# Performance work log

Hardware: AMD Instinct MI355X
Metric: run time of the kernel (lower is better)

Reference implementation:

```python
import jax, jax.numpy as jnp
import numpy as np

D_MODEL = 1024
N_HEADS = 16
D_K = D_MODEL // N_HEADS
THETA = 10000.0
NEG_INF = -1e30


def _rope_tables(token_positions, d_k, theta=THETA):
    # freqs[t, i] = t / theta**(2i/d_k), i in [0, d_k/2)
    exponent = jnp.arange(0, d_k, 2, dtype=jnp.float32)  # [d_k/2]
    inv_freq = 1.0 / theta ** (exponent / d_k)
    freqs = token_positions.astype(jnp.float32)[:, None] * inv_freq[None, :]  # [s, d_k/2]
    return jnp.cos(freqs), jnp.sin(freqs)


def _apply_rope(x, cos, sin):
    # x: [..., s, d_k]; interleaved pair rotation (pairs are (x[2i], x[2i+1]))
    x1 = x[..., 0::2]
    x2 = x[..., 1::2]
    r1 = x1 * cos - x2 * sin
    r2 = x1 * sin + x2 * cos
    return jnp.stack([r1, r2], axis=-1).reshape(x.shape)


def setup_inputs() -> dict:
    key = jax.random.key(0)
    ks = jax.random.split(key, 5)
    b, s = 2, 2048
    scale = np.sqrt(2.0 / (D_MODEL + D_MODEL))
    return {
        "x": jax.random.normal(ks[0], (b, s, D_MODEL), dtype=jnp.float32),
        "Wq": jax.random.normal(ks[1], (D_MODEL, D_MODEL), dtype=jnp.float32) * scale,
        "Wk": jax.random.normal(ks[2], (D_MODEL, D_MODEL), dtype=jnp.float32) * scale,
        "Wv": jax.random.normal(ks[3], (D_MODEL, D_MODEL), dtype=jnp.float32) * scale,
        "Wo": jax.random.normal(ks[4], (D_MODEL, D_MODEL), dtype=jnp.float32) * scale,
        "token_positions": jnp.arange(s, dtype=jnp.int64 if jax.config.jax_enable_x64 else jnp.int32),
    }


def reference(x, Wq, Wk, Wv, Wo, token_positions):
    b, s, _ = x.shape
    # QKV projections: weight stored [in, out]
    q = jnp.einsum('bsi,io->bso', x, Wq)
    k = jnp.einsum('bsi,io->bso', x, Wk)
    v = jnp.einsum('bsi,io->bso', x, Wv)
    # split heads: [b, h, s, d_k]
    q = q.reshape(b, s, N_HEADS, D_K).transpose(0, 2, 1, 3)
    k = k.reshape(b, s, N_HEADS, D_K).transpose(0, 2, 1, 3)
    v = v.reshape(b, s, N_HEADS, D_K).transpose(0, 2, 1, 3)
    # RoPE
    cos, sin = _rope_tables(token_positions, D_K)
    q = _apply_rope(q, cos, sin)
    k = _apply_rope(k, cos, sin)
    # causal attention with full materialized scores (faithful to source)
    scores = jnp.einsum('bhid,bhjd->bhij', q, k) / jnp.sqrt(jnp.float32(D_K))
    mask = jnp.tril(jnp.ones((s, s), dtype=bool))
    scores = jnp.where(mask, scores, NEG_INF)
    probs = jax.nn.softmax(scores, axis=-1)
    out = jnp.einsum('bhij,bhjd->bhid', probs, v)
    out = out.transpose(0, 2, 1, 3).reshape(b, s, D_MODEL)
    return jnp.einsum('bsi,io->bso', out, Wo)
```

## Files before the change

### kernel.cpp

```cpp
#include <hip/hip_runtime.h>
#include <hip/hip_bf16.h>
#include <cmath>

#define S_LEN 2048
#define DMODEL 1024
#define NHEADS 16
#define DK 64
#define BATCH 2
#define MTOT (BATCH * S_LEN)

using short8 = __attribute__((ext_vector_type(8))) short;
using floatx4 = __attribute__((ext_vector_type(4))) float;

__device__ __forceinline__ unsigned short f2b(float f) {
    union { float f; unsigned u; } v; v.f = f;
    unsigned r = v.u + 0x7fff + ((v.u >> 16) & 1);
    return (unsigned short)(r >> 16);
}

__device__ __forceinline__ unsigned pack2(float a, float b) {
    float2 t; t.x = a; t.y = b;
    __hip_bfloat162 h = __float22bfloat162_rn(t);
    union { __hip_bfloat162 h; unsigned u; } v; v.h = h;
    return v.u;
}

__device__ __forceinline__ void gload16(const void* g, void* l) {
    __builtin_amdgcn_global_load_lds(
        (const __attribute__((address_space(1))) unsigned int*)g,
        (__attribute__((address_space(3))) unsigned int*)l, 16, 0, 0);
}

__global__ __launch_bounds__(256) void prep_k(
    const float* __restrict__ x, unsigned short* __restrict__ xb,
    const int* __restrict__ tokpos, float* __restrict__ ct, float* __restrict__ st,
    const float* W0, const float* W1, const float* W2, const float* W3,
    unsigned short* T0, unsigned short* T1, unsigned short* T2, unsigned short* T3) {
    __shared__ float t[64][65];
    const int b = blockIdx.x;
    if (b < 2048) {
        int i = (b * 256 + threadIdx.x) * 8;
        float4 a = *(const float4*)(x + i);
        float4 bb = *(const float4*)(x + i + 4);
        short8 o;
        o[0] = f2b(a.x); o[1] = f2b(a.y); o[2] = f2b(a.z); o[3] = f2b(a.w);
        o[4] = f2b(bb.x); o[5] = f2b(bb.y); o[6] = f2b(bb.z); o[7] = f2b(bb.w);
        *(short8*)(xb + i) = o;
    } else if (b < 2304) {
        int idx = (b - 2048) * 256 + threadIdx.x;
        int si = idx >> 5;
        int ip = idx & 31;
        float pos = (float)tokpos[si];
        float inv_freq = powf(10000.0f, -(float)(2 * ip) / 64.0f);
        float ang = pos * inv_freq;
        ct[idx] = cosf(ang);
        st[idx] = sinf(ang);
    } else {
        int id = b - 2304;
        int z = id >> 8;
        int bx = id & 15, by = (id >> 4) & 15;
        const float* W = z == 0 ? W0 : z == 1 ? W1 : z == 2 ? W2 : W3;
        unsigned short* T = z == 0 ? T0 : z == 1 ? T1 : z == 2 ? T2 : T3;
        const bool perm = (z < 2);
        int n0 = bx * 64, k0 = by * 64;
        int rr = threadIdx.x >> 6, cc = threadIdx.x & 63;
#pragma unroll
        for (int r = 0; r < 16; r++) {
            int row = r * 4 + rr;
            t[row][cc] = W[(size_t)(k0 + row) * DMODEL + n0 + cc];
        }
        __syncthreads();
#pragma unroll
        for (int r = 0; r < 16; r++) {
            int row = r * 4 + rr;
            int drow = perm ? (((row & 1) ? 32 : 0) + (row >> 1)) : row;
            T[(size_t)(n0 + drow) * DMODEL + k0 + cc] = f2b(t[cc][row]);
        }
    }
}

__global__ __launch_bounds__(256) void vtrans_k(const unsigned short* __restrict__ V,
                                                unsigned short* __restrict__ Vt) {
    __shared__ unsigned short t[64][72];
    const int tid = threadIdx.x;
    const int s0 = blockIdx.x * 64, d0 = blockIdx.y * 64;
    const int bb = s0 >> 11;
#pragma unroll
    for (int it = 0; it < 4; it++) {
        int e = (it * 256 + tid) * 4;
        int r = e >> 6, c = e & 63;
        *(ushort4*)&t[r][c] = *(const ushort4*)(V + (size_t)(s0 + r) * DMODEL + d0 + c);
    }
    __syncthreads();
#pragma unroll
    for (int it = 0; it < 4; it++) {
        int e = (it * 256 + tid) * 4;
        int r = e >> 6, c = e & 63;
        ushort4 v;
        v.x = t[c + 0][r]; v.y = t[c + 1][r];
        v.z = t[c + 2][r]; v.w = t[c + 3][r];
        *(ushort4*)(Vt + (size_t)(bb * 1024 + d0 + r) * S_LEN + (s0 & (S_LEN - 1)) + c) = v;
    }
}

__global__ __launch_bounds__(256) void mm_k(
    const unsigned short* __restrict__ A,
    const unsigned short* __restrict__ Bt0, const unsigned short* __restrict__ Bt1,
    const unsigned short* __restrict__ Bt2,
    void* C0, void* C1, void* C2,
    const float* __restrict__ ct, const float* __restrict__ st, int kind) {
    __shared__ __align__(16) unsigned short blob[2][8192];

    const int z = blockIdx.z;
    const unsigned short* Bt = z == 0 ? Bt0 : z == 1 ? Bt1 : Bt2;
    void* C = z == 0 ? C0 : z == 1 ? C1 : C2;
    const int mode = (kind == 1) ? 0 : (z == 2 ? 3 : 1);
    const float qscale = (z == 0 && kind == 0) ? 0.18033688011112042f : 1.0f;

    const int tid = threadIdx.x;
    const int w = tid >> 6, lane = tid & 63;
    const int l15 = lane & 15, quad = lane >> 4;
    const int wr = w >> 1, wc = w & 1;
    const int m0 = blockIdx.x * 128, n0 = blockIdx.y * 128;

    floatx4 acc[4][4];
#pragma unroll
    for (int i = 0; i < 4; i++)
#pragma unroll
        for (int j = 0; j < 4; j++) acc[i][j] = (floatx4){0.f, 0.f, 0.f, 0.f};

    auto stage = [&](int buf, int k0) {
#pragma unroll
        for (int it = 0; it < 4; it++) {
            int g = it * 4 + w;
            const unsigned short* gp;
            if (g < 8)
                gp = A + (size_t)(m0 + g * 16 + l15) * DMODEL + k0 + quad * 8;
            else
                gp = Bt + (size_t)(n0 + (g - 8) * 16 + l15) * DMODEL + k0 + quad * 8;
            gload16(gp, (char*)&blob[buf][0] + g * 1024);
        }
    };

    stage(0, 0);
    for (int kt = 0; kt < DMODEL / 32; kt++) {
        const int b = kt & 1;
        __syncthreads();
        if (kt + 1 < DMODEL / 32) stage(b ^ 1, (kt + 1) * 32);

        const char* base = (const char*)&blob[b][0];
        short8 af[4], bfr[4];
#pragma unroll
        for (int i = 0; i < 4; i++)
            af[i] = *(const short8*)(base + ((wr * 4 + i) * 64 + lane) * 16);
#pragma unroll
        for (int j = 0; j < 4; j++)
            bfr[j] = *(const short8*)(base + 8192 + ((wc * 4 + j) * 64 + lane) * 16);
#pragma unroll
        for (int i = 0; i < 4; i++)
#pragma unroll
            for (int j = 0; j < 4; j++)
                acc[i][j] = __builtin_amdgcn_mfma_f32_16x16x32_bf16(af[i], bfr[j], acc[i][j], 0, 0, 0);
    }

#pragma unroll
    for (int i = 0; i < 4; i++) {
        const int rowb = m0 + wr * 64 + i * 16 + quad * 4;
        if (mode == 0) {
            float* Cf = (float*)C;
#pragma unroll
            for (int j = 0; j < 4; j++) {
                int colb = n0 + wc * 64 + j * 16 + l15;
#pragma unroll
                for (int r = 0; r < 4; r++)
                    Cf[(size_t)(rowb + r) * DMODEL + colb] = acc[i][j][r];
            }
        } else if (mode == 1) {
            unsigned short* Cb = (unsigned short*)C;
#pragma unroll
            for (int jh = 0; jh < 2; jh++) {
                int ip = jh * 16 + l15;
                int cole = n0 + wc * 64 + jh * 16 + l15;
#pragma unroll
                for (int r = 0; r < 4; r++) {
                    int row = rowb + r;
                    int si = row & (S_LEN - 1);
                    float c = ct[si * 32 + ip] * qscale;
                    float s = st[si * 32 + ip] * qscale;
                    float e = acc[i][jh][r];
                    float od = acc[i][jh + 2][r];
                    Cb[(size_t)row * DMODEL + cole] = f2b(e * c - od * s);
                    Cb[(size_t)row * DMODEL + cole + 32] = f2b(e * s + od * c);
                }
            }
        } else {
            unsigned short* Cb = (unsigned short*)C;
#pragma unroll
            for (int j = 0; j < 4; j++) {
                int colb = n0 + wc * 64 + j * 16 + l15;
#pragma unroll
                for (int r = 0; r < 4; r++)
                    Cb[(size_t)(rowb + r) * DMODEL + colb] = f2b(acc[i][j][r]);
            }
        }
    }
}

__global__ __launch_bounds__(512) void attn_k(const unsigned short* __restrict__ Q,
                                              const unsigned short* __restrict__ K,
                                              const unsigned short* __restrict__ Vt,
                                              unsigned short* __restrict__ O) {
    __shared__ __align__(16) unsigned short Kblob[2][4096];
    __shared__ __align__(16) unsigned short Vblob[2][4096];
    __shared__ __align__(16) unsigned short Ps[8][16 * 72];

    const int tid = threadIdx.x;
    const int w = tid >> 6, lane = tid & 63;
    const int l15 = lane & 15, quad = lane >> 4;
    const int idx = blockIdx.x;
    const int qt = 15 - (idx >> 5);
    const int bh = idx & 31;
    const int bb = bh >> 4, h = bh & 15;
    const int qbase = qt * 128 + w * 16;
    const int qrow = qbase + l15;

    const size_t qoff = (size_t)(bb * S_LEN + qbase + l15) * DMODEL + h * DK;
    short8 aq0 = *(const short8*)(Q + qoff + quad * 8);
    short8 aq1 = *(const short8*)(Q + qoff + 32 + quad * 8);

    floatx4 o[4];
#pragma unroll
    for (int f = 0; f < 4; f++) o[f] = (floatx4){0.f, 0.f, 0.f, 0.f};
    float mv = -1e30f, lv = 0.f;

    const unsigned short* Kb = K + (size_t)(bb * S_LEN) * DMODEL + h * DK;
    const unsigned short* Vb = Vt + (size_t)(bb * 1024 + h * DK) * S_LEN;
    unsigned short* ps = &Ps[w][0];

    auto stage = [&](int b, int kb) {
#pragma unroll
        for (int it = 0; it < 2; it++) {
            int g = it * 8 + w;
            if (g < 8) {
                const unsigned short* gp =
                    Kb + (size_t)(kb + (g >> 1) * 16 + l15) * DMODEL + (g & 1) * 32 + quad * 8;
                gload16(gp, (char*)&Kblob[b][0] + g * 1024);
            } else {
                int gv = g - 8;
                const unsigned short* gp =
                    Vb + (size_t)((gv >> 1) * 16 + l15) * S_LEN + kb + (gv & 1) * 32 + quad * 8;
                gload16(gp, (char*)&Vblob[b][0] + gv * 1024);
            }
        }
    };

    const int nkt = 2 * qt + 2;
    stage(0, 0);
    for (int kt = 0; kt < nkt; kt++) {
        const int b = kt & 1;
        const int kb = kt * 64;
        __syncthreads();
        if (kt + 1 < nkt) stage(b ^ 1, (kt + 1) * 64);

        const unsigned short* kbb = &Kblob[b][0];
        floatx4 c[4];
#pragma unroll
        for (int g = 0; g < 4; g++) {
            short8 kf0 = *(const short8*)(kbb + (g * 2 + 0) * 512 + lane * 8);
            short8 kf1 = *(const short8*)(kbb + (g * 2 + 1) * 512 + lane * 8);
            floatx4 t = {0.f, 0.f, 0.f, 0.f};
            t = __builtin_amdgcn_mfma_f32_16x16x32_bf16(kf0, aq0, t, 0, 0, 0);
            c[g] = __builtin_amdgcn_mfma_f32_16x16x32_bf16(kf1, aq1, t, 0, 0, 0);
        }

        float sv[16];
        if (kb + 63 <= qbase) {
#pragma unroll
            for (int g = 0; g < 4; g++)
#pragma unroll
                for (int r = 0; r < 4; r++) sv[g * 4 + r] = c[g][r];
        } else {
#pragma unroll
            for (int g = 0; g < 4; g++)
#pragma unroll
                for (int r = 0; r < 4; r++) {
                    int key = kb + g * 16 + quad * 4 + r;
                    sv[g * 4 + r] = (key <= qrow) ? c[g][r] : -1e30f;
                }
        }
        float mx = sv[0];
#pragma unroll
        for (int i = 1; i < 16; i++) mx = fmaxf(mx, sv[i]);
        mx = fmaxf(mx, __shfl_xor(mx, 16));
        mx = fmaxf(mx, __shfl_xor(mx, 32));
        float mnew = fmaxf(mv, mx);
        float alpha = exp2f(mv - mnew);
        mv = mnew;
        float p[16], psum = 0.f;
#pragma unroll
        for (int i = 0; i < 16; i++) {
            p[i] = exp2f(sv[i] - mnew);
            psum += p[i];
        }
        lv = lv * alpha + psum;

#pragma unroll
        for (int g = 0; g < 4; g++) {
            uint2 pk;
            pk.x = pack2(p[g * 4 + 0], p[g * 4 + 1]);
            pk.y = pack2(p[g * 4 + 2], p[g * 4 + 3]);
            *(uint2*)(ps + l15 * 72 + g * 16 + quad * 4) = pk;
        }
#pragma unroll
        for (int f = 0; f < 4; f++) {
            o[f][0] *= alpha; o[f][1] *= alpha;
            o[f][2] *= alpha; o[f][3] *= alpha;
        }
        short8 pf0 = *(const short8*)(ps + l15 * 72 + quad * 8);
        short8 pf1 = *(const short8*)(ps + l15 * 72 + 32 + quad * 8);
        const unsigned short* vbb = &Vblob[b][0];
#pragma unroll
        for (int f = 0; f < 4; f++) {
            short8 vf0 = *(const short8*)(vbb + (f * 2 + 0) * 512 + lane * 8);
            short8 vf1 = *(const short8*)(vbb + (f * 2 + 1) * 512 + lane * 8);
            o[f] = __builtin_amdgcn_mfma_f32_16x16x32_bf16(vf0, pf0, o[f], 0, 0, 0);
            o[f] = __builtin_amdgcn_mfma_f32_16x16x32_bf16(vf1, pf1, o[f], 0, 0, 0);
        }
    }

    lv += __shfl_xor(lv, 16);
    lv += __shfl_xor(lv, 32);
    float inv = 1.0f / lv;
    __syncthreads();
#pragma unroll
    for (int f = 0; f < 4; f++) {
        uint2 pk;
        pk.x = pack2(o[f][0] * inv, o[f][1] * inv);
        pk.y = pack2(o[f][2] * inv, o[f][3] * inv);
        *(uint2*)(ps + l15 * 72 + f * 16 + quad * 4) = pk;
    }
    short8 r0 = *(const short8*)(ps + l15 * 72 + quad * 8);
    short8 r1 = *(const short8*)(ps + l15 * 72 + 32 + quad * 8);
    size_t obase = (size_t)(bb * S_LEN + qbase + l15) * DMODEL + h * DK;
    *(short8*)(O + obase + quad * 8) = r0;
    *(short8*)(O + obase + 32 + quad * 8) = r1;
}

extern "C" void kernel_launch(void* const* d_in, const int* in_sizes, int n_in,
                              void* d_out, int out_size, void* d_ws,
                              size_t ws_size, hipStream_t stream) {
    const float* x = (const float*)d_in[0];
    const float* Wq = (const float*)d_in[1];
    const float* Wk = (const float*)d_in[2];
    const float* Wv = (const float*)d_in[3];
    const float* Wo = (const float*)d_in[4];
    const int* tokpos = (const int*)d_in[5];
    float* out = (float*)d_out;

    const size_t MD = (size_t)MTOT * DMODEL;
    const size_t WD = (size_t)DMODEL * DMODEL;
    unsigned short* xb = (unsigned short*)d_ws;
    unsigned short* Wqt = xb + MD;
    unsigned short* Wkt = Wqt + WD;
    unsigned short* Wvt = Wkt + WD;
    unsigned short* Wot = Wvt + WD;
    unsigned short* Q = Wot + WD;
    unsigned short* K = Q + MD;
    unsigned short* V = K + MD;
    unsigned short* Vt = V + MD;
    float* ct = (float*)(Vt + MD);
    float* st = ct + S_LEN * 32;
    unsigned short* O = V;

    prep_k<<<dim3(3328), dim3(256), 0, stream>>>(x, xb, tokpos, ct, st,
                                                 Wq, Wk, Wv, Wo, Wqt, Wkt, Wvt, Wot);

    mm_k<<<dim3(32, 8, 3), dim3(256), 0, stream>>>(xb, Wqt, Wkt, Wvt,
                                                   (void*)Q, (void*)K, (void*)V, ct, st, 0);
    vtrans_k<<<dim3(64, 16), dim3(256), 0, stream>>>(V, Vt);
    attn_k<<<dim3(512), dim3(512), 0, stream>>>(Q, K, Vt, O);
    mm_k<<<dim3(32, 8, 1), dim3(256), 0, stream>>>(O, Wot, Wot, Wot,
                                                   (void*)out, (void*)out, (void*)out, ct, st, 1);
}
```

Measured before the change: 212.3 us.

## Split-K the output projection into two bf16 partials plus an add kernel

The output projection GEMM is split along K into two halves run as separate grid z-slices. Each half writes a bf16 partial into the freed Q and K buffers, and a new elementwise kernel sums them into the fp32 output. This doubles the block count for that GEMM to improve CU occupancy and latency hiding. The cost is an extra launch, extra memory traffic for the partials, and lower output precision because the partials are rounded to bf16 before the sum.

```diff
diff --git a/kernel.cpp b/kernel.cpp
--- a/kernel.cpp
+++ b/kernel.cpp
@@ -16,6 +16,11 @@
     union { float f; unsigned u; } v; v.f = f;
     unsigned r = v.u + 0x7fff + ((v.u >> 16) & 1);
     return (unsigned short)(r >> 16);
+}
+
+__device__ __forceinline__ float b2f(unsigned short b) {
+    union { unsigned u; float f; } v; v.u = ((unsigned)b) << 16;
+    return v.f;
 }
 
 __device__ __forceinline__ unsigned pack2(float a, float b) {
@@ -103,6 +108,21 @@
     }
 }
 
+__global__ __launch_bounds__(256) void add_k(const unsigned short* __restrict__ p0,
+                                             const unsigned short* __restrict__ p1,
+                                             float* __restrict__ out) {
+    int i = (blockIdx.x * 256 + threadIdx.x) * 8;
+    short8 a = *(const short8*)(p0 + i);
+    short8 b = *(const short8*)(p1 + i);
+    float4 r0, r1;
+    r0.x = b2f(a[0]) + b2f(b[0]); r0.y = b2f(a[1]) + b2f(b[1]);
+    r0.z = b2f(a[2]) + b2f(b[2]); r0.w = b2f(a[3]) + b2f(b[3]);
+    r1.x = b2f(a[4]) + b2f(b[4]); r1.y = b2f(a[5]) + b2f(b[5]);
+    r1.z = b2f(a[6]) + b2f(b[6]); r1.w = b2f(a[7]) + b2f(b[7]);
+    *(float4*)(out + i) = r0;
+    *(float4*)(out + i + 4) = r1;
+}
+
 __global__ __launch_bounds__(256) void mm_k(
     const unsigned short* __restrict__ A,
     const unsigned short* __restrict__ Bt0, const unsigned short* __restrict__ Bt1,
@@ -114,7 +134,9 @@
     const int z = blockIdx.z;
     const unsigned short* Bt = z == 0 ? Bt0 : z == 1 ? Bt1 : Bt2;
     void* C = z == 0 ? C0 : z == 1 ? C1 : C2;
-    const int mode = (kind == 1) ? 0 : (z == 2 ? 3 : 1);
+    const int mode = (kind == 2) ? 3 : (z == 2 ? 3 : 1);
+    const int kbeg = (kind == 2) ? z * 512 : 0;
+    const int kend = (kind == 2) ? kbeg + 512 : DMODEL;
     const float qscale = (z == 0 && kind == 0) ? 0.18033688011112042f : 1.0f;
 
     const int tid = threadIdx.x;
@@ -142,11 +164,12 @@
         }
     };
 
-    stage(0, 0);
-    for (int kt = 0; kt < DMODEL / 32; kt++) {
+    const int niter = (kend - kbeg) / 32;
+    stage(0, kbeg);
+    for (int kt = 0; kt < niter; kt++) {
         const int b = kt & 1;
         __syncthreads();
-        if (kt + 1 < DMODEL / 32) stage(b ^ 1, (kt + 1) * 32);
+        if (kt + 1 < niter) stage(b ^ 1, kbeg + (kt + 1) * 32);
 
         const char* base = (const char*)&blob[b][0];
         short8 af[4], bfr[4];
@@ -166,16 +189,7 @@
 #pragma unroll
     for (int i = 0; i < 4; i++) {
         const int rowb = m0 + wr * 64 + i * 16 + quad * 4;
-        if (mode == 0) {
-            float* Cf = (float*)C;
-#pragma unroll
-            for (int j = 0; j < 4; j++) {
-                int colb = n0 + wc * 64 + j * 16 + l15;
-#pragma unroll
-                for (int r = 0; r < 4; r++)
-                    Cf[(size_t)(rowb + r) * DMODEL + colb] = acc[i][j][r];
-            }
-        } else if (mode == 1) {
+        if (mode == 1) {
             unsigned short* Cb = (unsigned short*)C;
 #pragma unroll
             for (int jh = 0; jh < 2; jh++) {
@@ -371,6 +385,8 @@
     float* ct = (float*)(Vt + MD);
     float* st = ct + S_LEN * 32;
     unsigned short* O = V;
+    unsigned short* P0 = Q;
+    unsigned short* P1 = K;
 
     prep_k<<<dim3(3328), dim3(256), 0, stream>>>(x, xb, tokpos, ct, st,
                                                  Wq, Wk, Wv, Wo, Wqt, Wkt, Wvt, Wot);
@@ -379,6 +395,7 @@
                                                    (void*)Q, (void*)K, (void*)V, ct, st, 0);
     vtrans_k<<<dim3(64, 16), dim3(256), 0, stream>>>(V, Vt);
     attn_k<<<dim3(512), dim3(512), 0, stream>>>(Q, K, Vt, O);
-    mm_k<<<dim3(32, 8, 1), dim3(256), 0, stream>>>(O, Wot, Wot, Wot,
-                                                   (void*)out, (void*)out, (void*)out, ct, st, 1);
-}
+    mm_k<<<dim3(32, 8, 2), dim3(256), 0, stream>>>(O, Wot, Wot, Wot,
+                                                   (void*)P0, (void*)P1, (void*)P1, ct, st, 2);
+    add_k<<<dim3(2048), dim3(256), 0, stream>>>(P0, P1, out);
+}
```

Result: slower. 223.9 us (+5.5%).
